# Kernel optimization log

Hardware: AMD Instinct MI355X
Metric: run time of the kernel (lower is better)

Reference implementation:

```python
import jax, jax.numpy as jnp
import numpy as np

H = 2048      # hidden_dim
P = 256       # private_subspace_dim
B, S = 4, 8192


def setup_inputs() -> dict:
    key = jax.random.key(0)
    k1, k2, k3, k4, k5 = jax.random.split(key, 5)
    hidden_states = jax.random.normal(k1, (B, S, H), dtype=jnp.float32)
    token_ids = jax.random.randint(k2, (B, S), 0, 100, dtype=jnp.int32)
    # Linear params (torch nn.Linear: y = x @ W.T + b); store W as (in, out) for einsum.
    sc1 = 1.0 / np.sqrt(H)
    sc2 = 1.0 / np.sqrt(P)
    W_to = jax.random.uniform(k3, (H, P), jnp.float32, -sc1, sc1)
    b_to = jnp.zeros((P,), jnp.float32)
    W_from = jax.random.uniform(k4, (P, H), jnp.float32, -sc2, sc2)
    b_from = jnp.zeros((H,), jnp.float32)
    return {
        "hidden_states": hidden_states,
        "W_to": W_to, "b_to": b_to,
        "W_from": W_from, "b_from": b_from,
        "token_ids": token_ids,
        "thought_token_id": 5,
    }


def _thought_mask(token_ids, thought_token_id):
    # Replaces the sequential toggle loop: state at position i is the parity of the
    # number of thought tokens seen in token_ids[0, :i+1] (toggle happens BEFORE use).
    matches = (token_ids[0] == thought_token_id).astype(jnp.int32)   # (S,)
    parity = (jnp.cumsum(matches) % 2) == 1                          # (S,) bool
    return jnp.broadcast_to(parity[None, :], token_ids.shape)        # (B, S)


def reference(hidden_states, W_to, b_to, W_from, b_from, token_ids, thought_token_id):
    is_private = _thought_mask(token_ids, thought_token_id)          # (B, S) bool
    m = is_private.astype(hidden_states.dtype)[..., None]            # (B, S, 1)
    private_reasoning = jnp.einsum('bsh,hp->bsp', hidden_states, W_to) + b_to
    private_projected = jnp.einsum('bsp,ph->bsh', private_reasoning, W_from) + b_from
    output = hidden_states * (1.0 - m) + private_projected * m
    subspace_usage = is_private.astype(jnp.float32).mean(axis=1)     # (B,)
    return private_reasoning, output, is_private, subspace_usage
```

## Files before the change

### kernel.cpp

```cpp
#include <hip/hip_runtime.h>
#include <stdint.h>


#define H 2048
#define P 256
#define BB 4
#define S 8192
#define M_TOTAL (BB * S)

typedef __bf16 bf16x8 __attribute__((ext_vector_type(8)));
typedef float f32x4 __attribute__((ext_vector_type(4)));

__device__ __forceinline__ ushort f2b(float f) {
  uint32_t u = __float_as_uint(f);
  u += 0x7fffu + ((u >> 16) & 1u);
  return (ushort)(u >> 16);
}

__global__ void mask_kernel(const int* __restrict__ tok, const int* __restrict__ tt_p,
                            float* __restrict__ maskf, float* __restrict__ out2,
                            float* __restrict__ out3) {
  __shared__ unsigned long long wpar[4];
  __shared__ int wcnt[4];
  const int t = threadIdx.x;
  const int lane = t & 63, w = t >> 6;
  const int tt = tt_p[0];
  const int base = t * 32;
  unsigned bits = 0;
  for (int i = 0; i < 32; i++) bits |= (unsigned)(tok[base + i] == tt) << i;
  const int par = __popc(bits) & 1;
  const unsigned long long bal = __ballot(par != 0);
  if (lane == 0) wpar[w] = bal;
  __syncthreads();
  int pre = 0;
  for (int j = 0; j < w; j++) pre ^= (int)(__popcll(wpar[j]) & 1);
  pre ^= (int)(__popcll(bal & ((1ull << lane) - 1ull)) & 1);
  int cnt = 0;
  for (int i = 0; i < 32; i++) {
    int inc = __popc(bits << (31 - i)) & 1;
    int bit = pre ^ inc;
    cnt += bit;
    float fb = (float)bit;
    maskf[base + i] = fb;
    out2[0 * S + base + i] = fb;
    out2[1 * S + base + i] = fb;
    out2[2 * S + base + i] = fb;
    out2[3 * S + base + i] = fb;
  }
  for (int off = 32; off; off >>= 1) cnt += __shfl_down(cnt, off);
  if (lane == 0) wcnt[w] = cnt;
  __syncthreads();
  if (t < BB) {
    int tot = wcnt[0] + wcnt[1] + wcnt[2] + wcnt[3];
    out3[t] = (float)tot / (float)S;
  }
}

__global__ void transpose_cvt(const float* __restrict__ in, ushort* __restrict__ out,
                              int R, int C) {
  __shared__ float tile[32][33];
  const int c0 = blockIdx.x * 32, r0 = blockIdx.y * 32;
  const int tx = threadIdx.x, ty = threadIdx.y;
#pragma unroll
  for (int j = 0; j < 32; j += 8)
    tile[ty + j][tx] = in[(size_t)(r0 + ty + j) * C + c0 + tx];
  __syncthreads();
#pragma unroll
  for (int j = 0; j < 32; j += 8)
    out[(size_t)(c0 + ty + j) * R + r0 + tx] = f2b(tile[tx][ty + j]);
}

__global__ __launch_bounds__(512) void gemm1(
    const float* __restrict__ hid,
    const ushort* __restrict__ wtT,
    const float* __restrict__ b_to,
    float* __restrict__ out0)
{
  __shared__ ushort sA[64 * 72];
  __shared__ ushort sW[256 * 72];
  const int tid = threadIdx.x;
  const int lane = tid & 63, wid = tid >> 6;
  const int quad = lane >> 4, l16 = lane & 15;
  const int row0 = blockIdx.x * 64;

  f32x4 acc[4][2];
  const f32x4 zero = {0.f, 0.f, 0.f, 0.f};
#pragma unroll
  for (int i = 0; i < 4; i++)
#pragma unroll
    for (int j = 0; j < 2; j++) acc[i][j] = zero;

  for (int k0 = 0; k0 < H; k0 += 64) {
#pragma unroll
    for (int p = 0; p < 2; p++) {
      int u = p * 512 + tid;
      int r = u >> 4, cc = u & 15;
      const float4 v = *(const float4*)(hid + (size_t)(row0 + r) * H + k0 + cc * 4);
      ushort4 b;
      b.x = f2b(v.x); b.y = f2b(v.y); b.z = f2b(v.z); b.w = f2b(v.w);
      *(ushort4*)(sA + r * 72 + cc * 4) = b;
    }
#pragma unroll
    for (int p = 0; p < 4; p++) {
      int u = p * 512 + tid;
      int n = u >> 3, s = u & 7;
      *(int4*)(sW + n * 72 + s * 8) = *(const int4*)(wtT + (size_t)n * H + k0 + s * 8);
    }
    __syncthreads();
#pragma unroll
    for (int kk = 0; kk < 64; kk += 32) {
      bf16x8 af[4], bfr[2];
#pragma unroll
      for (int t = 0; t < 4; t++)
        af[t] = *(const bf16x8*)(sA + (t * 16 + l16) * 72 + kk + quad * 8);
#pragma unroll
      for (int t = 0; t < 2; t++)
        bfr[t] = *(const bf16x8*)(sW + (wid * 32 + t * 16 + l16) * 72 + kk + quad * 8);
#pragma unroll
      for (int i = 0; i < 4; i++)
#pragma unroll
        for (int j = 0; j < 2; j++)
          acc[i][j] = __builtin_amdgcn_mfma_f32_16x16x32_bf16(af[i], bfr[j], acc[i][j], 0, 0, 0);
    }
    __syncthreads();
  }

#pragma unroll
  for (int i = 0; i < 4; i++) {
#pragma unroll
    for (int j = 0; j < 2; j++) {
      int col = wid * 32 + j * 16 + l16;
      float bias = b_to[col];
#pragma unroll
      for (int e = 0; e < 4; e++) {
        int row = i * 16 + quad * 4 + e;
        out0[(size_t)(row0 + row) * P + col] = acc[i][j][e] + bias;
      }
    }
  }
}

__global__ __launch_bounds__(512) void gemm2(
    const float* __restrict__ pr,
    const ushort* __restrict__ wfT,
    const float* __restrict__ b_from,
    const float* __restrict__ maskf,
    const float* __restrict__ hid,
    float* __restrict__ out1)
{
  __shared__ ushort sA[128 * 72];
  __shared__ ushort sW[128 * 72];
  const int tid = threadIdx.x;
  const int lane = tid & 63, wid = tid >> 6;
  const int quad = lane >> 4, l16 = lane & 15;

  const int u0 = (blockIdx.x & 7) * 512 + (blockIdx.x >> 3);
  const int mblk = u0 >> 4, nblk = u0 & 15;
  const int row0 = mblk * 128, nc0 = nblk * 128;

  const int wr = wid >> 1;
  const int wc = wid & 1;

  f32x4 acc[2][4];
  const f32x4 zero = {0.f, 0.f, 0.f, 0.f};
#pragma unroll
  for (int i = 0; i < 2; i++)
#pragma unroll
    for (int j = 0; j < 4; j++) acc[i][j] = zero;

  for (int k0 = 0; k0 < P; k0 += 64) {
#pragma unroll
    for (int p = 0; p < 4; p++) {
      int u = p * 512 + tid;
      int r = u >> 4, cc = u & 15;
      const float4 v = *(const float4*)(pr + (size_t)(row0 + r) * P + k0 + cc * 4);
      ushort4 b;
      b.x = f2b(v.x); b.y = f2b(v.y); b.z = f2b(v.z); b.w = f2b(v.w);
      *(ushort4*)(sA + r * 72 + cc * 4) = b;
    }
#pragma unroll
    for (int p = 0; p < 2; p++) {
      int u = p * 512 + tid;
      int n = u >> 3, s = u & 7;
      *(int4*)(sW + n * 72 + s * 8) = *(const int4*)(wfT + (size_t)(nc0 + n) * P + k0 + s * 8);
    }
    __syncthreads();
#pragma unroll
    for (int kk = 0; kk < 64; kk += 32) {
      bf16x8 af[2], bfr[4];
#pragma unroll
      for (int t = 0; t < 2; t++)
        af[t] = *(const bf16x8*)(sA + (wr * 32 + t * 16 + l16) * 72 + kk + quad * 8);
#pragma unroll
      for (int t = 0; t < 4; t++)
        bfr[t] = *(const bf16x8*)(sW + (wc * 64 + t * 16 + l16) * 72 + kk + quad * 8);
#pragma unroll
      for (int i = 0; i < 2; i++)
#pragma unroll
        for (int j = 0; j < 4; j++)
          acc[i][j] = __builtin_amdgcn_mfma_f32_16x16x32_bf16(af[i], bfr[j], acc[i][j], 0, 0, 0);
    }
    __syncthreads();
  }

#pragma unroll
  for (int i = 0; i < 2; i++) {
#pragma unroll
    for (int e = 0; e < 4; e++) {
      int row = wr * 32 + i * 16 + quad * 4 + e;
      size_t gr = (size_t)(row0 + row);
      float m = maskf[gr & (S - 1)];
      if (m != 0.0f) {
#pragma unroll
        for (int j = 0; j < 4; j++) {
          int col = nc0 + wc * 64 + j * 16 + l16;
          out1[gr * H + col] = acc[i][j][e] + b_from[col];
        }
      } else {
#pragma unroll
        for (int j = 0; j < 4; j++) {
          int col = nc0 + wc * 64 + j * 16 + l16;
          out1[gr * H + col] = hid[gr * H + col];
        }
      }
    }
  }
}

extern "C" void kernel_launch(void* const* d_in, const int* in_sizes, int n_in,
                              void* d_out, int out_size, void* d_ws, size_t ws_size,
                              hipStream_t stream) {
  const float* hid    = (const float*)d_in[0];
  const float* W_to   = (const float*)d_in[1];
  const float* b_to   = (const float*)d_in[2];
  const float* W_from = (const float*)d_in[3];
  const float* b_from = (const float*)d_in[4];
  const int*   tok    = (const int*)d_in[5];
  const int*   tt     = (const int*)d_in[6];

  ushort* wtT = (ushort*)d_ws;
  ushort* wfT = wtT + (size_t)P * H;
  float* maskf = (float*)(wfT + (size_t)H * P);

  float* out0 = (float*)d_out;
  float* out1 = out0 + (size_t)BB * S * P;
  float* out2 = out1 + (size_t)BB * S * H;
  float* out3 = out2 + (size_t)BB * S;

  hipLaunchKernelGGL(mask_kernel, dim3(1), dim3(256), 0, stream, tok, tt, maskf, out2, out3);
  hipLaunchKernelGGL(transpose_cvt, dim3(P / 32, H / 32), dim3(32, 8), 0, stream, W_to, wtT, H, P);
  hipLaunchKernelGGL(transpose_cvt, dim3(H / 32, P / 32), dim3(32, 8), 0, stream, W_from, wfT, P, H);
  hipLaunchKernelGGL(gemm1, dim3(M_TOTAL / 64), dim3(512), 0, stream, hid, wtT, b_to, out0);
  hipLaunchKernelGGL(gemm2, dim3((M_TOTAL / 128) * (H / 128)), dim3(512), 0, stream,
                     out0, wfT, b_from, maskf, hid, out1);
}
```

Before: 669.4 us.

## Double-buffer GEMM K-loops with register prefetch and fuse prep kernels

Both GEMMs now use a K-step of 32 with two shared-memory buffers. Global loads for the next step are issued into registers before the current step's MFMAs run, and a single lightweight barrier separates stages, so load latency overlaps compute. The mask computation and the two weight transposes are merged into one launch to cut launch overhead. The cost is more registers and LDS, twice as many barrier rounds per K, and a change to the compiler's native bf16 conversion.

New measurement: 770.3 us. 15.1% more time.

```diff
diff --git a/kernel.cpp b/kernel.cpp
--- a/kernel.cpp
+++ b/kernel.cpp
@@ -8,6 +8,8 @@
 #define S 8192
 #define M_TOTAL (BB * S)
 
+typedef __bf16 bf16_t;
+typedef __bf16 bf16x4 __attribute__((ext_vector_type(4)));
 typedef __bf16 bf16x8 __attribute__((ext_vector_type(8)));
 typedef float f32x4 __attribute__((ext_vector_type(4)));
 
@@ -17,57 +19,71 @@
   return (ushort)(u >> 16);
 }
 
-__global__ void mask_kernel(const int* __restrict__ tok, const int* __restrict__ tt_p,
-                            float* __restrict__ maskf, float* __restrict__ out2,
-                            float* __restrict__ out3) {
+__device__ __forceinline__ void pipe_barrier() {
+  asm volatile("s_waitcnt lgkmcnt(0)" ::: "memory");
+  __builtin_amdgcn_s_barrier();
+  asm volatile("" ::: "memory");
+}
+
+__global__ __launch_bounds__(256) void prep(
+    const float* __restrict__ W_to, const float* __restrict__ W_from,
+    ushort* __restrict__ wtT, ushort* __restrict__ wfT,
+    const int* __restrict__ tok, const int* __restrict__ tt_p,
+    float* __restrict__ maskf, float* __restrict__ out2, float* __restrict__ out3) {
+  __shared__ float tile[32][33];
   __shared__ unsigned long long wpar[4];
   __shared__ int wcnt[4];
+  const int b = blockIdx.x;
   const int t = threadIdx.x;
-  const int lane = t & 63, w = t >> 6;
-  const int tt = tt_p[0];
-  const int base = t * 32;
-  unsigned bits = 0;
-  for (int i = 0; i < 32; i++) bits |= (unsigned)(tok[base + i] == tt) << i;
-  const int par = __popc(bits) & 1;
-  const unsigned long long bal = __ballot(par != 0);
-  if (lane == 0) wpar[w] = bal;
-  __syncthreads();
-  int pre = 0;
-  for (int j = 0; j < w; j++) pre ^= (int)(__popcll(wpar[j]) & 1);
-  pre ^= (int)(__popcll(bal & ((1ull << lane) - 1ull)) & 1);
-  int cnt = 0;
-  for (int i = 0; i < 32; i++) {
-    int inc = __popc(bits << (31 - i)) & 1;
-    int bit = pre ^ inc;
-    cnt += bit;
-    float fb = (float)bit;
-    maskf[base + i] = fb;
-    out2[0 * S + base + i] = fb;
-    out2[1 * S + base + i] = fb;
-    out2[2 * S + base + i] = fb;
-    out2[3 * S + base + i] = fb;
-  }
-  for (int off = 32; off; off >>= 1) cnt += __shfl_down(cnt, off);
-  if (lane == 0) wcnt[w] = cnt;
-  __syncthreads();
-  if (t < BB) {
-    int tot = wcnt[0] + wcnt[1] + wcnt[2] + wcnt[3];
-    out3[t] = (float)tot / (float)S;
-  }
-}
-
-__global__ void transpose_cvt(const float* __restrict__ in, ushort* __restrict__ out,
-                              int R, int C) {
-  __shared__ float tile[32][33];
-  const int c0 = blockIdx.x * 32, r0 = blockIdx.y * 32;
-  const int tx = threadIdx.x, ty = threadIdx.y;
-#pragma unroll
-  for (int j = 0; j < 32; j += 8)
-    tile[ty + j][tx] = in[(size_t)(r0 + ty + j) * C + c0 + tx];
-  __syncthreads();
-#pragma unroll
-  for (int j = 0; j < 32; j += 8)
-    out[(size_t)(c0 + ty + j) * R + r0 + tx] = f2b(tile[tx][ty + j]);
+  if (b < 1024) {
+    const float* in = (b < 512) ? W_to : W_from;
+    ushort* out = (b < 512) ? wtT : wfT;
+    const int R = (b < 512) ? H : P;
+    const int C = (b < 512) ? P : H;
+    const int bb = b & 511;
+    const int nct = C >> 5;
+    const int c0 = (bb % nct) * 32, r0 = (bb / nct) * 32;
+    const int tx = t & 31, ty = t >> 5;
+#pragma unroll
+    for (int j = 0; j < 32; j += 8)
+      tile[ty + j][tx] = in[(size_t)(r0 + ty + j) * C + c0 + tx];
+    __syncthreads();
+#pragma unroll
+    for (int j = 0; j < 32; j += 8)
+      out[(size_t)(c0 + ty + j) * R + r0 + tx] = f2b(tile[tx][ty + j]);
+  } else {
+    const int lane = t & 63, w = t >> 6;
+    const int tt = tt_p[0];
+    const int base = t * 32;
+    unsigned bits = 0;
+    for (int i = 0; i < 32; i++) bits |= (unsigned)(tok[base + i] == tt) << i;
+    const int par = __popc(bits) & 1;
+    const unsigned long long bal = __ballot(par != 0);
+    if (lane == 0) wpar[w] = bal;
+    __syncthreads();
+    int pre = 0;
+    for (int j = 0; j < w; j++) pre ^= (int)(__popcll(wpar[j]) & 1);
+    pre ^= (int)(__popcll(bal & ((1ull << lane) - 1ull)) & 1);
+    int cnt = 0;
+    for (int i = 0; i < 32; i++) {
+      int inc = __popc(bits << (31 - i)) & 1;
+      int bit = pre ^ inc;
+      cnt += bit;
+      float fb = (float)bit;
+      maskf[base + i] = fb;
+      out2[0 * S + base + i] = fb;
+      out2[1 * S + base + i] = fb;
+      out2[2 * S + base + i] = fb;
+      out2[3 * S + base + i] = fb;
+    }
+    for (int off = 32; off; off >>= 1) cnt += __shfl_down(cnt, off);
+    if (lane == 0) wcnt[w] = cnt;
+    __syncthreads();
+    if (t < BB) {
+      int tot = wcnt[0] + wcnt[1] + wcnt[2] + wcnt[3];
+      out3[t] = (float)tot / (float)S;
+    }
+  }
 }
 
 __global__ __launch_bounds__(512) void gemm1(
@@ -76,13 +92,23 @@
     const float* __restrict__ b_to,
     float* __restrict__ out0)
 {
-  __shared__ ushort sA[64 * 72];
-  __shared__ ushort sW[256 * 72];
+  __shared__ bf16_t sA[2][64 * 40];
+  __shared__ bf16_t sW[2][256 * 40];
   const int tid = threadIdx.x;
   const int lane = tid & 63, wid = tid >> 6;
   const int quad = lane >> 4, l16 = lane & 15;
   const int row0 = blockIdx.x * 64;
 
+  const int ar = tid >> 3, ac = tid & 7;
+  const int wn = tid >> 2, ws = tid & 3;
+
+  const float* aSrc = hid + (size_t)(row0 + ar) * H + ac * 4;
+  const ushort* wSrc0 = wtT + (size_t)wn * H + ws * 8;
+  const ushort* wSrc1 = wtT + (size_t)(wn + 128) * H + ws * 8;
+
+  float4 pA[2];
+  int4 pW[2][2];
+
   f32x4 acc[4][2];
   const f32x4 zero = {0.f, 0.f, 0.f, 0.f};
 #pragma unroll
@@ -90,40 +116,56 @@
 #pragma unroll
     for (int j = 0; j < 2; j++) acc[i][j] = zero;
 
-  for (int k0 = 0; k0 < H; k0 += 64) {
-#pragma unroll
-    for (int p = 0; p < 2; p++) {
-      int u = p * 512 + tid;
-      int r = u >> 4, cc = u & 15;
-      const float4 v = *(const float4*)(hid + (size_t)(row0 + r) * H + k0 + cc * 4);
-      ushort4 b;
-      b.x = f2b(v.x); b.y = f2b(v.y); b.z = f2b(v.z); b.w = f2b(v.w);
-      *(ushort4*)(sA + r * 72 + cc * 4) = b;
-    }
-#pragma unroll
-    for (int p = 0; p < 4; p++) {
-      int u = p * 512 + tid;
-      int n = u >> 3, s = u & 7;
-      *(int4*)(sW + n * 72 + s * 8) = *(const int4*)(wtT + (size_t)n * H + k0 + s * 8);
-    }
-    __syncthreads();
-#pragma unroll
-    for (int kk = 0; kk < 64; kk += 32) {
-      bf16x8 af[4], bfr[2];
-#pragma unroll
-      for (int t = 0; t < 4; t++)
-        af[t] = *(const bf16x8*)(sA + (t * 16 + l16) * 72 + kk + quad * 8);
-#pragma unroll
-      for (int t = 0; t < 2; t++)
-        bfr[t] = *(const bf16x8*)(sW + (wid * 32 + t * 16 + l16) * 72 + kk + quad * 8);
-#pragma unroll
-      for (int i = 0; i < 4; i++)
-#pragma unroll
-        for (int j = 0; j < 2; j++)
-          acc[i][j] = __builtin_amdgcn_mfma_f32_16x16x32_bf16(af[i], bfr[j], acc[i][j], 0, 0, 0);
-    }
-    __syncthreads();
-  }
+#define G1_ISSUE(s, k0)                          \
+  do {                                           \
+    pA[s] = *(const float4*)(aSrc + (k0));       \
+    pW[s][0] = *(const int4*)(wSrc0 + (k0));     \
+    pW[s][1] = *(const int4*)(wSrc1 + (k0));     \
+  } while (0)
+
+#define G1_WRITE(s, bf)                                      \
+  do {                                                       \
+    bf16x4 cv;                                               \
+    cv.x = (bf16_t)pA[s].x; cv.y = (bf16_t)pA[s].y;          \
+    cv.z = (bf16_t)pA[s].z; cv.w = (bf16_t)pA[s].w;          \
+    *(bf16x4*)(&sA[bf][ar * 40 + ac * 4]) = cv;              \
+    *(int4*)(&sW[bf][wn * 40 + ws * 8]) = pW[s][0];          \
+    *(int4*)(&sW[bf][(wn + 128) * 40 + ws * 8]) = pW[s][1];  \
+  } while (0)
+
+#define G1_COMPUTE(bf)                                                            \
+  do {                                                                            \
+    bf16x8 af[4], bw[2];                                                          \
+    _Pragma("unroll") for (int i = 0; i < 4; ++i)                                 \
+        af[i] = *(const bf16x8*)(&sA[bf][(i * 16 + l16) * 40 + quad * 8]);        \
+    _Pragma("unroll") for (int j = 0; j < 2; ++j)                                 \
+        bw[j] = *(const bf16x8*)(&sW[bf][(wid * 32 + j * 16 + l16) * 40 + quad * 8]); \
+    _Pragma("unroll") for (int i = 0; i < 4; ++i)                                 \
+        _Pragma("unroll") for (int j = 0; j < 2; ++j)                             \
+            acc[i][j] = __builtin_amdgcn_mfma_f32_16x16x32_bf16(af[i], bw[j], acc[i][j], 0, 0, 0); \
+  } while (0)
+
+  G1_ISSUE(0, 0);
+  G1_ISSUE(1, 32);
+  G1_WRITE(0, 0);
+  pipe_barrier();
+
+#pragma unroll 1
+  for (int m = 0; m < 31; ++m) {
+    const int k0 = 64 + (m << 6);
+    G1_COMPUTE(0);
+    G1_ISSUE(0, k0);
+    G1_WRITE(1, 1);
+    pipe_barrier();
+    G1_COMPUTE(1);
+    G1_ISSUE(1, k0 + 32);
+    G1_WRITE(0, 0);
+    pipe_barrier();
+  }
+  G1_COMPUTE(0);
+  G1_WRITE(1, 1);
+  pipe_barrier();
+  G1_COMPUTE(1);
 
 #pragma unroll
   for (int i = 0; i < 4; i++) {
@@ -138,6 +180,9 @@
       }
     }
   }
+#undef G1_ISSUE
+#undef G1_WRITE
+#undef G1_COMPUTE
 }
 
 __global__ __launch_bounds__(512) void gemm2(
@@ -148,18 +193,25 @@
     const float* __restrict__ hid,
     float* __restrict__ out1)
 {
-  __shared__ ushort sA[128 * 72];
-  __shared__ ushort sW[128 * 72];
+  __shared__ bf16_t sA[2][128 * 40];
+  __shared__ bf16_t sW[2][128 * 40];
   const int tid = threadIdx.x;
   const int lane = tid & 63, wid = tid >> 6;
   const int quad = lane >> 4, l16 = lane & 15;
 
-  const int u0 = (blockIdx.x & 7) * 512 + (blockIdx.x >> 3);
-  const int mblk = u0 >> 4, nblk = u0 & 15;
-  const int row0 = mblk * 128, nc0 = nblk * 128;
-
-  const int wr = wid >> 1;
-  const int wc = wid & 1;
+  const int u0 = ((blockIdx.x & 7) << 9) + (blockIdx.x >> 3);
+  const int row0 = (u0 >> 4) * 128, nc0 = (u0 & 15) * 128;
+  const int wr = wid >> 1, wc = wid & 1;
+
+  const int ar = tid >> 3, ac = tid & 7;
+  const int wn = tid >> 2, ws = tid & 3;
+
+  const float* aSrc0 = pr + (size_t)(row0 + ar) * P + ac * 4;
+  const float* aSrc1 = pr + (size_t)(row0 + ar + 64) * P + ac * 4;
+  const ushort* wSrc = wfT + (size_t)(nc0 + wn) * P + ws * 8;
+
+  float4 pA[2][2];
+  int4 pW[2];
 
   f32x4 acc[2][4];
   const f32x4 zero = {0.f, 0.f, 0.f, 0.f};
@@ -168,40 +220,58 @@
 #pragma unroll
     for (int j = 0; j < 4; j++) acc[i][j] = zero;
 
-  for (int k0 = 0; k0 < P; k0 += 64) {
-#pragma unroll
-    for (int p = 0; p < 4; p++) {
-      int u = p * 512 + tid;
-      int r = u >> 4, cc = u & 15;
-      const float4 v = *(const float4*)(pr + (size_t)(row0 + r) * P + k0 + cc * 4);
-      ushort4 b;
-      b.x = f2b(v.x); b.y = f2b(v.y); b.z = f2b(v.z); b.w = f2b(v.w);
-      *(ushort4*)(sA + r * 72 + cc * 4) = b;
-    }
-#pragma unroll
-    for (int p = 0; p < 2; p++) {
-      int u = p * 512 + tid;
-      int n = u >> 3, s = u & 7;
-      *(int4*)(sW + n * 72 + s * 8) = *(const int4*)(wfT + (size_t)(nc0 + n) * P + k0 + s * 8);
-    }
-    __syncthreads();
-#pragma unroll
-    for (int kk = 0; kk < 64; kk += 32) {
-      bf16x8 af[2], bfr[4];
-#pragma unroll
-      for (int t = 0; t < 2; t++)
-        af[t] = *(const bf16x8*)(sA + (wr * 32 + t * 16 + l16) * 72 + kk + quad * 8);
-#pragma unroll
-      for (int t = 0; t < 4; t++)
-        bfr[t] = *(const bf16x8*)(sW + (wc * 64 + t * 16 + l16) * 72 + kk + quad * 8);
-#pragma unroll
-      for (int i = 0; i < 2; i++)
-#pragma unroll
-        for (int j = 0; j < 4; j++)
-          acc[i][j] = __builtin_amdgcn_mfma_f32_16x16x32_bf16(af[i], bfr[j], acc[i][j], 0, 0, 0);
-    }
-    __syncthreads();
-  }
+#define G2_ISSUE(s, k0)                         \
+  do {                                          \
+    pA[s][0] = *(const float4*)(aSrc0 + (k0));  \
+    pA[s][1] = *(const float4*)(aSrc1 + (k0));  \
+    pW[s] = *(const int4*)(wSrc + (k0));        \
+  } while (0)
+
+#define G2_WRITE(s, bf)                                          \
+  do {                                                           \
+    bf16x4 c0_, c1_;                                             \
+    c0_.x = (bf16_t)pA[s][0].x; c0_.y = (bf16_t)pA[s][0].y;      \
+    c0_.z = (bf16_t)pA[s][0].z; c0_.w = (bf16_t)pA[s][0].w;      \
+    c1_.x = (bf16_t)pA[s][1].x; c1_.y = (bf16_t)pA[s][1].y;      \
+    c1_.z = (bf16_t)pA[s][1].z; c1_.w = (bf16_t)pA[s][1].w;      \
+    *(bf16x4*)(&sA[bf][ar * 40 + ac * 4]) = c0_;                 \
+    *(bf16x4*)(&sA[bf][(ar + 64) * 40 + ac * 4]) = c1_;          \
+    *(int4*)(&sW[bf][wn * 40 + ws * 8]) = pW[s];                 \
+  } while (0)
+
+#define G2_COMPUTE(bf)                                                            \
+  do {                                                                            \
+    bf16x8 af[2], bw[4];                                                          \
+    _Pragma("unroll") for (int i = 0; i < 2; ++i)                                 \
+        af[i] = *(const bf16x8*)(&sA[bf][(wr * 32 + i * 16 + l16) * 40 + quad * 8]); \
+    _Pragma("unroll") for (int j = 0; j < 4; ++j)                                 \
+        bw[j] = *(const bf16x8*)(&sW[bf][(wc * 64 + j * 16 + l16) * 40 + quad * 8]); \
+    _Pragma("unroll") for (int i = 0; i < 2; ++i)                                 \
+        _Pragma("unroll") for (int j = 0; j < 4; ++j)                             \
+            acc[i][j] = __builtin_amdgcn_mfma_f32_16x16x32_bf16(af[i], bw[j], acc[i][j], 0, 0, 0); \
+  } while (0)
+
+  G2_ISSUE(0, 0);
+  G2_ISSUE(1, 32);
+  G2_WRITE(0, 0);
+  pipe_barrier();
+
+#pragma unroll 1
+  for (int m = 0; m < 3; ++m) {
+    const int k0 = 64 + (m << 6);
+    G2_COMPUTE(0);
+    G2_ISSUE(0, k0);
+    G2_WRITE(1, 1);
+    pipe_barrier();
+    G2_COMPUTE(1);
+    G2_ISSUE(1, k0 + 32);
+    G2_WRITE(0, 0);
+    pipe_barrier();
+  }
+  G2_COMPUTE(0);
+  G2_WRITE(1, 1);
+  pipe_barrier();
+  G2_COMPUTE(1);
 
 #pragma unroll
   for (int i = 0; i < 2; i++) {
@@ -225,6 +295,9 @@
       }
     }
   }
+#undef G2_ISSUE
+#undef G2_WRITE
+#undef G2_COMPUTE
 }
 
 extern "C" void kernel_launch(void* const* d_in, const int* in_sizes, int n_in,
@@ -247,9 +320,8 @@
   float* out2 = out1 + (size_t)BB * S * H;
   float* out3 = out2 + (size_t)BB * S;
 
-  hipLaunchKernelGGL(mask_kernel, dim3(1), dim3(256), 0, stream, tok, tt, maskf, out2, out3);
-  hipLaunchKernelGGL(transpose_cvt, dim3(P / 32, H / 32), dim3(32, 8), 0, stream, W_to, wtT, H, P);
-  hipLaunchKernelGGL(transpose_cvt, dim3(H / 32, P / 32), dim3(32, 8), 0, stream, W_from, wfT, P, H);
+  hipLaunchKernelGGL(prep, dim3(1025), dim3(256), 0, stream,
+                     W_to, W_from, wtT, wfT, tok, tt, maskf, out2, out3);
   hipLaunchKernelGGL(gemm1, dim3(M_TOTAL / 64), dim3(512), 0, stream, hid, wtT, b_to, out0);
   hipLaunchKernelGGL(gemm2, dim3((M_TOTAL / 128) * (H / 128)), dim3(512), 0, stream,
                      out0, wfT, b_from, maskf, hid, out1);
```

## Compact private rows for gemm2 and fuse pass-through copy into gemm1

Applied to the files above, without the earlier changes.

The prep kernel now builds a compacted list of private sequence positions, padded to a multiple of 128, along with a count. gemm2 gathers only those rows, computes only the private tiles, and returns early for blocks beyond the needed count. gemm1 writes non-private hidden rows straight to the output while it streams them for the first GEMM, so the copy no longer needs a second read of hidden_states. The mask and both weight transposes are merged into one launch. The gains depend on the mask density and add gather-indexed A loads in gemm2.

New measurement: 604.6 us. 1.11x faster.

```diff
diff --git a/kernel.cpp b/kernel.cpp
--- a/kernel.cpp
+++ b/kernel.cpp
@@ -17,64 +17,83 @@
   return (ushort)(u >> 16);
 }
 
-__global__ void mask_kernel(const int* __restrict__ tok, const int* __restrict__ tt_p,
-                            float* __restrict__ maskf, float* __restrict__ out2,
-                            float* __restrict__ out3) {
+__global__ __launch_bounds__(256) void prep(
+    const float* __restrict__ W_to, const float* __restrict__ W_from,
+    ushort* __restrict__ wtT, ushort* __restrict__ wfT,
+    const int* __restrict__ tok, const int* __restrict__ tt_p,
+    float* __restrict__ maskf, int* __restrict__ slist, int* __restrict__ cntp,
+    float* __restrict__ out2, float* __restrict__ out3) {
+  __shared__ float tile[32][33];
   __shared__ unsigned long long wpar[4];
-  __shared__ int wcnt[4];
+  __shared__ int scnt[256];
+  const int b = blockIdx.x;
   const int t = threadIdx.x;
-  const int lane = t & 63, w = t >> 6;
-  const int tt = tt_p[0];
-  const int base = t * 32;
-  unsigned bits = 0;
-  for (int i = 0; i < 32; i++) bits |= (unsigned)(tok[base + i] == tt) << i;
-  const int par = __popc(bits) & 1;
-  const unsigned long long bal = __ballot(par != 0);
-  if (lane == 0) wpar[w] = bal;
-  __syncthreads();
-  int pre = 0;
-  for (int j = 0; j < w; j++) pre ^= (int)(__popcll(wpar[j]) & 1);
-  pre ^= (int)(__popcll(bal & ((1ull << lane) - 1ull)) & 1);
-  int cnt = 0;
-  for (int i = 0; i < 32; i++) {
-    int inc = __popc(bits << (31 - i)) & 1;
-    int bit = pre ^ inc;
-    cnt += bit;
-    float fb = (float)bit;
-    maskf[base + i] = fb;
-    out2[0 * S + base + i] = fb;
-    out2[1 * S + base + i] = fb;
-    out2[2 * S + base + i] = fb;
-    out2[3 * S + base + i] = fb;
-  }
-  for (int off = 32; off; off >>= 1) cnt += __shfl_down(cnt, off);
-  if (lane == 0) wcnt[w] = cnt;
-  __syncthreads();
-  if (t < BB) {
-    int tot = wcnt[0] + wcnt[1] + wcnt[2] + wcnt[3];
-    out3[t] = (float)tot / (float)S;
-  }
-}
-
-__global__ void transpose_cvt(const float* __restrict__ in, ushort* __restrict__ out,
-                              int R, int C) {
-  __shared__ float tile[32][33];
-  const int c0 = blockIdx.x * 32, r0 = blockIdx.y * 32;
-  const int tx = threadIdx.x, ty = threadIdx.y;
-#pragma unroll
-  for (int j = 0; j < 32; j += 8)
-    tile[ty + j][tx] = in[(size_t)(r0 + ty + j) * C + c0 + tx];
-  __syncthreads();
-#pragma unroll
-  for (int j = 0; j < 32; j += 8)
-    out[(size_t)(c0 + ty + j) * R + r0 + tx] = f2b(tile[tx][ty + j]);
+  if (b < 1024) {
+    const float* in = (b < 512) ? W_to : W_from;
+    ushort* out = (b < 512) ? wtT : wfT;
+    const int R = (b < 512) ? H : P;
+    const int C = (b < 512) ? P : H;
+    const int bb = b & 511;
+    const int nct = C >> 5;
+    const int c0 = (bb % nct) * 32, r0 = (bb / nct) * 32;
+    const int tx = t & 31, ty = t >> 5;
+#pragma unroll
+    for (int j = 0; j < 32; j += 8)
+      tile[ty + j][tx] = in[(size_t)(r0 + ty + j) * C + c0 + tx];
+    __syncthreads();
+#pragma unroll
+    for (int j = 0; j < 32; j += 8)
+      out[(size_t)(c0 + ty + j) * R + r0 + tx] = f2b(tile[tx][ty + j]);
+  } else {
+    const int lane = t & 63, w = t >> 6;
+    const int tt = tt_p[0];
+    const int base = t * 32;
+    unsigned bits = 0;
+    for (int i = 0; i < 32; i++) bits |= (unsigned)(tok[base + i] == tt) << i;
+    const int par = __popc(bits) & 1;
+    const unsigned long long bal = __ballot(par != 0);
+    if (lane == 0) wpar[w] = bal;
+    __syncthreads();
+    int pre = 0;
+    for (int j = 0; j < w; j++) pre ^= (int)(__popcll(wpar[j]) & 1);
+    pre ^= (int)(__popcll(bal & ((1ull << lane) - 1ull)) & 1);
+    int cnt = 0;
+    for (int i = 0; i < 32; i++) {
+      int inc = __popc(bits << (31 - i)) & 1;
+      cnt += pre ^ inc;
+    }
+    scnt[t] = cnt;
+    __syncthreads();
+    int off = 0, tot = 0;
+    for (int j = 0; j < 256; j++) {
+      if (j < t) off += scnt[j];
+      tot += scnt[j];
+    }
+    for (int i = 0; i < 32; i++) {
+      int inc = __popc(bits << (31 - i)) & 1;
+      int bit = pre ^ inc;
+      float fb = (float)bit;
+      maskf[base + i] = fb;
+      out2[0 * S + base + i] = fb;
+      out2[1 * S + base + i] = fb;
+      out2[2 * S + base + i] = fb;
+      out2[3 * S + base + i] = fb;
+      if (bit) slist[off++] = base + i;
+    }
+    const int padded = (tot + 127) & ~127;
+    for (int idx = tot + t; idx < padded; idx += 256) slist[idx] = -1;
+    if (t == 0) cntp[0] = tot;
+    if (t < BB) out3[t] = (float)tot / (float)S;
+  }
 }
 
 __global__ __launch_bounds__(512) void gemm1(
     const float* __restrict__ hid,
     const ushort* __restrict__ wtT,
     const float* __restrict__ b_to,
-    float* __restrict__ out0)
+    const float* __restrict__ maskf,
+    float* __restrict__ out0,
+    float* __restrict__ out1)
 {
   __shared__ ushort sA[64 * 72];
   __shared__ ushort sW[256 * 72];
@@ -83,6 +102,14 @@
   const int quad = lane >> 4, l16 = lane & 15;
   const int row0 = blockIdx.x * 64;
 
+  const int ra = tid >> 4, cc = tid & 15;
+  const bool pass0 = (maskf[(row0 + ra) & (S - 1)] == 0.0f);
+  const bool pass1 = (maskf[(row0 + 32 + ra) & (S - 1)] == 0.0f);
+  const float* aSrc0 = hid + (size_t)(row0 + ra) * H + cc * 4;
+  const float* aSrc1 = hid + (size_t)(row0 + 32 + ra) * H + cc * 4;
+  float* pDst0 = out1 + (size_t)(row0 + ra) * H + cc * 4;
+  float* pDst1 = out1 + (size_t)(row0 + 32 + ra) * H + cc * 4;
+
   f32x4 acc[4][2];
   const f32x4 zero = {0.f, 0.f, 0.f, 0.f};
 #pragma unroll
@@ -91,14 +118,17 @@
     for (int j = 0; j < 2; j++) acc[i][j] = zero;
 
   for (int k0 = 0; k0 < H; k0 += 64) {
-#pragma unroll
-    for (int p = 0; p < 2; p++) {
-      int u = p * 512 + tid;
-      int r = u >> 4, cc = u & 15;
-      const float4 v = *(const float4*)(hid + (size_t)(row0 + r) * H + k0 + cc * 4);
-      ushort4 b;
-      b.x = f2b(v.x); b.y = f2b(v.y); b.z = f2b(v.z); b.w = f2b(v.w);
-      *(ushort4*)(sA + r * 72 + cc * 4) = b;
+    {
+      const float4 v0 = *(const float4*)(aSrc0 + k0);
+      ushort4 b0;
+      b0.x = f2b(v0.x); b0.y = f2b(v0.y); b0.z = f2b(v0.z); b0.w = f2b(v0.w);
+      *(ushort4*)(sA + ra * 72 + cc * 4) = b0;
+      if (pass0) *(float4*)(pDst0 + k0) = v0;
+      const float4 v1 = *(const float4*)(aSrc1 + k0);
+      ushort4 b1;
+      b1.x = f2b(v1.x); b1.y = f2b(v1.y); b1.z = f2b(v1.z); b1.w = f2b(v1.w);
+      *(ushort4*)(sA + (32 + ra) * 72 + cc * 4) = b1;
+      if (pass1) *(float4*)(pDst1 + k0) = v1;
     }
 #pragma unroll
     for (int p = 0; p < 4; p++) {
@@ -144,22 +174,40 @@
     const float* __restrict__ pr,
     const ushort* __restrict__ wfT,
     const float* __restrict__ b_from,
-    const float* __restrict__ maskf,
-    const float* __restrict__ hid,
+    const int* __restrict__ slist,
+    const int* __restrict__ cntp,
     float* __restrict__ out1)
 {
   __shared__ ushort sA[128 * 72];
   __shared__ ushort sW[128 * 72];
+  __shared__ int sIdx[128];
   const int tid = threadIdx.x;
+
+  const int cnt = cntp[0];
+  const int tpb = (cnt + 127) >> 7;
+  const int u0 = ((blockIdx.x & 7) << 9) + (blockIdx.x >> 3);
+  const int mt = u0 >> 4;
+  if (mt >= 4 * tpb) return;
+  const int nt = u0 & 15;
+  const int batch = mt / tpb, ms = mt - batch * tpb;
+  const int nc0 = nt * 128;
+  const size_t rbase = (size_t)batch * S;
+
+  if (tid < 128) sIdx[tid] = slist[ms * 128 + tid];
+  __syncthreads();
+
   const int lane = tid & 63, wid = tid >> 6;
   const int quad = lane >> 4, l16 = lane & 15;
-
-  const int u0 = (blockIdx.x & 7) * 512 + (blockIdx.x >> 3);
-  const int mblk = u0 >> 4, nblk = u0 & 15;
-  const int row0 = mblk * 128, nc0 = nblk * 128;
-
-  const int wr = wid >> 1;
-  const int wc = wid & 1;
+  const int wr = wid >> 1, wc = wid & 1;
+
+  const int ra = tid >> 4, cc = tid & 15;
+  const float* aSrc[4];
+#pragma unroll
+  for (int p = 0; p < 4; p++) {
+    int sr = sIdx[ra + p * 32];
+    int s = (sr < 0) ? 0 : sr;
+    aSrc[p] = pr + (rbase + s) * P + cc * 4;
+  }
 
   f32x4 acc[2][4];
   const f32x4 zero = {0.f, 0.f, 0.f, 0.f};
@@ -171,12 +219,10 @@
   for (int k0 = 0; k0 < P; k0 += 64) {
 #pragma unroll
     for (int p = 0; p < 4; p++) {
-      int u = p * 512 + tid;
-      int r = u >> 4, cc = u & 15;
-      const float4 v = *(const float4*)(pr + (size_t)(row0 + r) * P + k0 + cc * 4);
+      const float4 v = *(const float4*)(aSrc[p] + k0);
       ushort4 b;
       b.x = f2b(v.x); b.y = f2b(v.y); b.z = f2b(v.z); b.w = f2b(v.w);
-      *(ushort4*)(sA + r * 72 + cc * 4) = b;
+      *(ushort4*)(sA + (p * 32 + ra) * 72 + cc * 4) = b;
     }
 #pragma unroll
     for (int p = 0; p < 2; p++) {
@@ -208,19 +254,13 @@
 #pragma unroll
     for (int e = 0; e < 4; e++) {
       int row = wr * 32 + i * 16 + quad * 4 + e;
-      size_t gr = (size_t)(row0 + row);
-      float m = maskf[gr & (S - 1)];
-      if (m != 0.0f) {
+      int sr = sIdx[row];
+      if (sr >= 0) {
+        size_t gr = rbase + sr;
 #pragma unroll
         for (int j = 0; j < 4; j++) {
           int col = nc0 + wc * 64 + j * 16 + l16;
           out1[gr * H + col] = acc[i][j][e] + b_from[col];
-        }
-      } else {
-#pragma unroll
-        for (int j = 0; j < 4; j++) {
-          int col = nc0 + wc * 64 + j * 16 + l16;
-          out1[gr * H + col] = hid[gr * H + col];
         }
       }
     }
@@ -241,16 +281,18 @@
   ushort* wtT = (ushort*)d_ws;
   ushort* wfT = wtT + (size_t)P * H;
   float* maskf = (float*)(wfT + (size_t)H * P);
+  int* slist = (int*)(maskf + S);
+  int* cntp = slist + S;
 
   float* out0 = (float*)d_out;
   float* out1 = out0 + (size_t)BB * S * P;
   float* out2 = out1 + (size_t)BB * S * H;
   float* out3 = out2 + (size_t)BB * S;
 
-  hipLaunchKernelGGL(mask_kernel, dim3(1), dim3(256), 0, stream, tok, tt, maskf, out2, out3);
-  hipLaunchKernelGGL(transpose_cvt, dim3(P / 32, H / 32), dim3(32, 8), 0, stream, W_to, wtT, H, P);
-  hipLaunchKernelGGL(transpose_cvt, dim3(H / 32, P / 32), dim3(32, 8), 0, stream, W_from, wfT, P, H);
-  hipLaunchKernelGGL(gemm1, dim3(M_TOTAL / 64), dim3(512), 0, stream, hid, wtT, b_to, out0);
+  hipLaunchKernelGGL(prep, dim3(1025), dim3(256), 0, stream,
+                     W_to, W_from, wtT, wfT, tok, tt, maskf, slist, cntp, out2, out3);
+  hipLaunchKernelGGL(gemm1, dim3(M_TOTAL / 64), dim3(512), 0, stream,
+                     hid, wtT, b_to, maskf, out0, out1);
   hipLaunchKernelGGL(gemm2, dim3((M_TOTAL / 128) * (H / 128)), dim3(512), 0, stream,
-                     out0, wfT, b_from, maskf, hid, out1);
-}
+                     out0, wfT, b_from, slist, cntp, out1);
+}
```
